# Performance work log

Measured on AMD Instinct MI355X. Metric: run time of the kernel, lower is better.

Reference implementation:

```python
import jax, jax.numpy as jnp
import numpy as np

N_NODES = 50000
N_EDGES = 320000
B = 4096          # subgraph batch: users/items/subg nodes
IN_N = 64         # in_nfeats
IN_E = 16         # in_efeats
OUT_E = 2 * IN_E  # out_edge_feats = in_efeats*2
H = 4             # num_heads
D = 64            # latent dim per layer (latent_dim=[64,64])
L = 2             # num EGAT layers


def setup_inputs() -> dict:
    key = jax.random.key(0)
    ks = iter(jax.random.split(key, 48))
    def nrm(shape, s=0.05):
        return jax.random.normal(next(ks), shape, dtype=jnp.float32) * s
    inp = {}
    inp['x'] = jax.random.normal(next(ks), (N_NODES, IN_N), dtype=jnp.float32)
    inp['efeat'] = jax.random.normal(next(ks), (N_EDGES, IN_E), dtype=jnp.float32)
    inp['efeat2'] = jax.random.normal(next(ks), (N_EDGES, IN_N), dtype=jnp.float32)
    inp['edge_mask'] = (jax.random.uniform(next(ks), (N_EDGES,)) > 0.1).astype(jnp.float32)
    inp['edge_mask2'] = (jax.random.uniform(next(ks), (N_EDGES,)) > 0.1).astype(jnp.float32)
    inp['src'] = jax.random.randint(next(ks), (N_EDGES,), 0, N_NODES, dtype=jnp.int32)
    inp['dst'] = jax.random.randint(next(ks), (N_EDGES,), 0, N_NODES, dtype=jnp.int32)
    inp['user_idx'] = jnp.arange(0, B, dtype=jnp.int32)          # ntype==0
    inp['item_idx'] = jnp.arange(B, 2 * B, dtype=jnp.int32)      # ntype==1
    inp['subg_idx'] = jnp.arange(2 * B, 3 * B, dtype=jnp.int32)  # ntype==-1
    # stacked per-layer EGAT params (layer dims identical since IN_N == D)
    inp['loc_wni'] = nrm((L, D, H * OUT_E))
    inp['loc_wnj'] = nrm((L, D, H * OUT_E))
    inp['loc_we'] = nrm((L, IN_E, H * OUT_E))
    inp['loc_attn'] = nrm((L, H, OUT_E))
    inp['loc_wnode'] = nrm((L, D, H * D))
    inp['agg1_w'] = nrm((L, H * D, D))
    inp['agg1_b'] = jnp.zeros((L, D), jnp.float32)
    inp['glob_wni'] = nrm((L, D, H * OUT_E))
    inp['glob_wnj'] = nrm((L, D, H * OUT_E))
    inp['glob_we'] = nrm((L, IN_N, H * OUT_E))
    inp['glob_attn'] = nrm((L, H, OUT_E))
    inp['glob_wnode'] = nrm((L, D, H * D))
    inp['agg2_w'] = nrm((L, H * D, D))
    inp['agg2_b'] = jnp.zeros((L, D), jnp.float32)
    inp['w1_ui'] = nrm((2 * L * D, 128))
    inp['b1_ui'] = jnp.zeros((128,), jnp.float32)
    inp['w1_sg'] = nrm((L * D, 128))
    inp['b1_sg'] = jnp.zeros((128,), jnp.float32)
    inp['w2_ui'] = nrm((128, 1))
    inp['b2_ui'] = jnp.zeros((1,), jnp.float32)
    inp['w2_sg'] = nrm((128, 1))
    inp['b2_sg'] = jnp.zeros((1,), jnp.float32)
    return inp


def _egat(x, e, norm, src, dst, wni, wnj, we, attn, wnode):
    # edge feature: f_ij = LeakyReLU(W_ni x_i + W_nj x_j + W_e e_ij), slope 0.2 (DGL EGATConv)
    f = (x @ wni)[src] + (x @ wnj)[dst] + e @ we            # (E, H*OUT_E)
    f = jax.nn.leaky_relu(f.reshape(-1, H, OUT_E), 0.2)
    scores = jnp.einsum('ehd,hd->eh', f, attn)              # (E, H)
    # edge softmax over incoming edges of each dst node
    m = jax.ops.segment_max(scores, dst, num_segments=N_NODES)
    m = jnp.where(jnp.isfinite(m), m, 0.0)
    ex = jnp.exp(scores - m[dst])
    denom = jax.ops.segment_sum(ex, dst, num_segments=N_NODES)
    a = ex / (denom[dst] + 1e-9)
    a = a * norm[:, None]                                    # per-edge norm (edge mask) weighting
    fn = (x @ wnode).reshape(-1, H, D)                       # (N, H, D)
    msg = fn[src] * a[:, :, None]                            # (E, H, D)
    out = jax.ops.segment_sum(msg, dst, num_segments=N_NODES)
    return out, a


def reference(x, efeat, efeat2, edge_mask, edge_mask2, src, dst, user_idx, item_idx, subg_idx,
              loc_wni, loc_wnj, loc_we, loc_attn, loc_wnode, agg1_w, agg1_b,
              glob_wni, glob_wnj, glob_we, glob_attn, glob_wnode, agg2_w, agg2_b,
              w1_ui, b1_ui, w1_sg, b1_sg, w2_ui, b2_ui, w2_sg, b2_sg):
    h = x
    ui_states, sg_states = [], []
    for l in range(L):
        out, _ = _egat(h, efeat, edge_mask, src, dst,
                       loc_wni[l], loc_wnj[l], loc_we[l], loc_attn[l], loc_wnode[l])
        h = jax.nn.elu(out.reshape(N_NODES, H * D) @ agg1_w[l] + agg1_b[l])
        ui_states.append(h)
        out, _ = _egat(h, efeat2, edge_mask2, src, dst,
                       glob_wni[l], glob_wnj[l], glob_we[l], glob_attn[l], glob_wnode[l])
        h = jax.nn.leaky_relu(out.reshape(N_NODES, H * D) @ agg2_w[l] + agg2_b[l], 0.01)
        sg_states.append(h)
    ui = jnp.concatenate(ui_states, axis=1)   # (N, L*D)
    sg = jnp.concatenate(sg_states, axis=1)   # (N, L*D)
    ui_x = jnp.concatenate([ui[user_idx], ui[item_idx]], axis=1)  # (B, 2*L*D)
    sg_x = sg[subg_idx]                                           # (B, L*D)
    ui_h = jax.nn.relu(ui_x @ w1_ui + b1_ui)  # dropout is identity in eval
    sg_h = jax.nn.relu(sg_x @ w1_sg + b1_sg)
    ui_out = jax.nn.sigmoid(ui_h @ w2_ui + b2_ui)[:, 0]
    sg_out = jax.nn.sigmoid(sg_h @ w2_sg + b2_sg)[:, 0]
    return (sg_out, ui_out)
```

## Files before the change

### kernel.cpp

```cpp
#include <hip/hip_runtime.h>
#include <math.h>

#define NN 50000
#define NE 320000
#define BATCH 4096

typedef __bf16 bf16x8 __attribute__((ext_vector_type(8)));
typedef float floatx4 __attribute__((ext_vector_type(4)));
typedef unsigned short ushort;
typedef unsigned int uint;

__device__ __forceinline__ float lrelu02(float x) { return x > 0.f ? x : 0.2f * x; }
__device__ __forceinline__ float b2f(ushort h) { return __uint_as_float(((uint)h) << 16); }
__device__ __forceinline__ float b2f_lo(uint u) { return __uint_as_float(u << 16); }
__device__ __forceinline__ float b2f_hi(uint u) { return __uint_as_float(u & 0xffff0000u); }
__device__ __forceinline__ ushort f2b(float x) {
    uint u = __float_as_uint(x);
    return (ushort)((u + 0x7fffu + ((u >> 16) & 1u)) >> 16);
}
__device__ __forceinline__ uint pk2(float a, float b) {
    return (uint)f2b(a) | ((uint)f2b(b) << 16);
}

template <int GLOB>
__global__ __launch_bounds__(512, 6) void score_frag(
    const float* __restrict__ ef,
    const ushort* __restrict__ Bfrag,
    const ushort* __restrict__ hb,
    const int* __restrict__ srcv, const int* __restrict__ dstv,
    const int* __restrict__ pos,
    const float* __restrict__ attn, float* __restrict__ scv)
{
    constexpr int KTOT = GLOB ? 192 : 160;
    constexpr int NR = KTOT / 32;
    constexpr int EFR = GLOB ? 2 : 1;
    constexpr int LDA = GLOB ? 64 : 16;
    __shared__ __align__(16) ushort As[128 * KTOT];
    const int tid = threadIdx.x;
    const int w = tid >> 6, lane = tid & 63;
    const int quad = lane >> 4, l16 = lane & 15;
    const int row = (blockIdx.x << 7) + 16 * w + l16;

    const int s_n = srcv[row];
    const int d_n = dstv[row];
    const int prow = pos[row];

    bf16x8 bfr[NR];
#pragma unroll
    for (int rnd = 0; rnd < EFR; rnd++) {
        uint4 av = make_uint4(0u, 0u, 0u, 0u);
        int k0 = rnd * 32 + quad * 8;
        if (GLOB || quad < 2) {
            const float* ap = ef + (size_t)row * LDA + k0;
            float4 f0 = *(const float4*)ap;
            float4 f1 = *(const float4*)(ap + 4);
            av.x = pk2(f0.x, f0.y);
            av.y = pk2(f0.z, f0.w);
            av.z = pk2(f1.x, f1.y);
            av.w = pk2(f1.z, f1.w);
        }
        *(uint4*)&bfr[rnd] = av;
    }
#pragma unroll
    for (int rr = 0; rr < 2; rr++)
        bfr[EFR + rr] = *(const bf16x8*)(hb + (size_t)s_n * 64 + rr * 32 + quad * 8);
#pragma unroll
    for (int rr = 0; rr < 2; rr++)
        bfr[EFR + 2 + rr] = *(const bf16x8*)(hb + (size_t)d_n * 64 + rr * 32 + quad * 8);

    for (int i = tid; i < 128 * KTOT / 8; i += 512)
        *(uint4*)(As + (size_t)i * 8) = *(const uint4*)(Bfrag + (size_t)i * 8);
    __syncthreads();

    floatx4 acc[8];
#pragma unroll
    for (int c = 0; c < 8; c++)
#pragma unroll
        for (int r = 0; r < 4; r++) acc[c][r] = 0.f;

#pragma unroll
    for (int rnd = 0; rnd < NR; rnd++) {
#pragma unroll
        for (int c = 0; c < 8; c++) {
            bf16x8 afr = *(const bf16x8*)(As + ((size_t)(c * NR + rnd) * 64 + lane) * 8);
            acc[c] = __builtin_amdgcn_mfma_f32_16x16x32_bf16(afr, bfr[rnd], acc[c], 0, 0, 0);
        }
    }

    float ph[4] = {0.f, 0.f, 0.f, 0.f};
#pragma unroll
    for (int c = 0; c < 8; c++) {
        int fbase = 16 * c + quad * 4;
        float4 at4 = *(const float4*)(attn + fbase);
        float v = lrelu02(acc[c][0]) * at4.x;
        v = fmaf(lrelu02(acc[c][1]), at4.y, v);
        v = fmaf(lrelu02(acc[c][2]), at4.z, v);
        v = fmaf(lrelu02(acc[c][3]), at4.w, v);
        ph[fbase >> 5] += v;
    }
#pragma unroll
    for (int h = 0; h < 4; h++) {
        ph[h] += __shfl_xor(ph[h], 16);
        ph[h] += __shfl_xor(ph[h], 32);
    }
    if (quad == 0)
        *(float4*)(scv + (size_t)prow * 4) = make_float4(ph[0], ph[1], ph[2], ph[3]);
}

__global__ __launch_bounds__(256) void gemm_agg(
    const ushort* __restrict__ A, int M,
    const ushort* __restrict__ Bt,
    const float* __restrict__ bias, int act,
    ushort* __restrict__ outb)
{
    __shared__ __align__(16) ushort As[64 * 32];
    __shared__ __align__(16) ushort Bs[64 * 32];
    const int tid = threadIdx.x;
    const int row0 = blockIdx.x << 6;
    const int w = tid >> 6, lane = tid & 63;
    const int quad = lane >> 4, l16 = lane & 15;
    const int arow = tid >> 2, c0 = (tid & 3) << 3;
    const int agrow = row0 + arow;

    floatx4 acc[4];
#pragma unroll
    for (int c = 0; c < 4; c++)
#pragma unroll
        for (int r = 0; r < 4; r++) acc[c][r] = 0.f;

    for (int kt = 0; kt < 256; kt += 32) {
        uint4 av = make_uint4(0u, 0u, 0u, 0u);
        if (agrow < M)
            av = *(const uint4*)(A + (size_t)agrow * 256 + kt + c0);
        *(uint4*)(As + arow * 32 + c0) = av;
        {
            int bn = tid >> 2, bk = (tid & 3) << 3;
            *(uint4*)(Bs + bn * 32 + bk) = *(const uint4*)(Bt + (size_t)bn * 256 + kt + bk);
        }
        __syncthreads();
        bf16x8 af = *(const bf16x8*)(As + (16 * w + l16) * 32 + quad * 8);
#pragma unroll
        for (int c = 0; c < 4; c++) {
            bf16x8 bfv = *(const bf16x8*)(Bs + (16 * c + l16) * 32 + quad * 8);
            acc[c] = __builtin_amdgcn_mfma_f32_16x16x32_bf16(af, bfv, acc[c], 0, 0, 0);
        }
        if (kt + 32 < 256) __syncthreads();
    }
#pragma unroll
    for (int r = 0; r < 4; r++) {
        int gr = row0 + 16 * w + quad * 4 + r;
        if (gr < M) {
#pragma unroll
            for (int c = 0; c < 4; c++) {
                int col = 16 * c + l16;
                float v = acc[c][r] + bias[col];
                if (act == 0) v = v > 0.f ? v : (__expf(v) - 1.f);
                else          v = v > 0.f ? v : 0.01f * v;
                outb[(size_t)gr * 64 + col] = f2b(v);
            }
        }
    }
}

__global__ void k_count(const int* __restrict__ dst, int* __restrict__ deg, int E)
{
    for (int i = blockIdx.x * blockDim.x + threadIdx.x; i < E; i += gridDim.x * blockDim.x)
        atomicAdd(&deg[dst[i]], 1);
}

__global__ __launch_bounds__(256) void scan_local(
    const int* __restrict__ deg, int* __restrict__ rowptr, int* __restrict__ partials, int N)
{
    __shared__ int sd[256];
    int tid = threadIdx.x;
    int i = blockIdx.x * 256 + tid;
    int v = (i < N) ? deg[i] : 0;
    sd[tid] = v; __syncthreads();
#pragma unroll
    for (int off = 1; off < 256; off <<= 1) {
        int t = (tid >= off) ? sd[tid - off] : 0;
        __syncthreads();
        sd[tid] += t;
        __syncthreads();
    }
    if (i < N) rowptr[i] = sd[tid] - v;
    if (tid == 255) partials[blockIdx.x] = sd[255];
}

__global__ __launch_bounds__(256) void scan_partials(int* __restrict__ partials, int nb)
{
    __shared__ int sd[256];
    int tid = threadIdx.x;
    int v = (tid < nb) ? partials[tid] : 0;
    sd[tid] = v; __syncthreads();
#pragma unroll
    for (int off = 1; off < 256; off <<= 1) {
        int t = (tid >= off) ? sd[tid - off] : 0;
        __syncthreads();
        sd[tid] += t;
        __syncthreads();
    }
    if (tid < nb) partials[tid] = sd[tid] - v;
}

__global__ void scan_add(int* __restrict__ rowptr, const int* __restrict__ partials, int N, int E)
{
    int i = blockIdx.x * 256 + threadIdx.x;
    if (i < N) rowptr[i] += partials[i >> 8];
    if (i == 0) rowptr[N] = E;
}

__global__ void k_scatter(const int* __restrict__ dst, const int* __restrict__ rowptr,
                          int* __restrict__ cnt, int* __restrict__ eidx, int E)
{
    for (int i = blockIdx.x * blockDim.x + threadIdx.x; i < E; i += gridDim.x * blockDim.x) {
        int d = dst[i];
        int p = rowptr[d] + atomicAdd(&cnt[d], 1);
        eidx[p] = i;
    }
}

__global__ void k_sort_buckets(const int* __restrict__ rowptr, int* __restrict__ eidx, int N)
{
    int n = blockIdx.x * blockDim.x + threadIdx.x;
    if (n >= N) return;
    int beg = rowptr[n], end = rowptr[n + 1];
    for (int i = beg + 1; i < end; i++) {
        int v = eidx[i];
        int j = i - 1;
        while (j >= beg && eidx[j] > v) { eidx[j + 1] = eidx[j]; j--; }
        eidx[j + 1] = v;
    }
}

__global__ void k_perm_small(const int* __restrict__ eidx, const int* __restrict__ src,
                             const float* __restrict__ m1, const float* __restrict__ m2,
                             int* __restrict__ srcp, float* __restrict__ m1p,
                             float* __restrict__ m2p, int* __restrict__ pos, int E)
{
    int p = blockIdx.x * blockDim.x + threadIdx.x;
    if (p < E) {
        int e = eidx[p];
        srcp[p] = src[e];
        m1p[p] = m1[e];
        m2p[p] = m2[e];
        pos[e] = p;
    }
}

__global__ void k_cvt(const float* __restrict__ in, ushort* __restrict__ out, int n)
{
    for (int i = blockIdx.x * blockDim.x + threadIdx.x; i < n; i += gridDim.x * blockDim.x)
        out[i] = f2b(in[i]);
}

__global__ void k_prep_score_all(const float* __restrict__ loc_we, const float* __restrict__ glob_we,
                                 const float* __restrict__ loc_wni, const float* __restrict__ glob_wni,
                                 const float* __restrict__ loc_wnj, const float* __restrict__ glob_wnj,
                                 ushort* __restrict__ B)
{
    int idx = blockIdx.x * 256 + threadIdx.x;
    if (idx >= 4 * 24576) return;
    int e = idx / 24576, rem = idx % 24576;
    int layer = e >> 1, gl = e & 1;
    int KTOT = gl ? 192 : 160;
    int NR = KTOT / 32;
    int ef_end = gl ? 64 : 32;
    int ef_real = gl ? 64 : 16;
    if (rem >= 128 * KTOT) return;
    int j = rem & 7, lane = (rem >> 3) & 63, t = rem >> 9;
    int c = t / NR, rnd = t % NR;
    int m = 16 * c + (lane & 15);
    int k = 32 * rnd + (lane >> 4) * 8 + j;
    const float* we  = (gl ? glob_we  + layer * 64 * 128 : loc_we  + layer * 16 * 128);
    const float* wni = (gl ? glob_wni : loc_wni) + layer * 64 * 128;
    const float* wnj = (gl ? glob_wnj : loc_wnj) + layer * 64 * 128;
    float v;
    if (k < ef_end)            v = (k < ef_real) ? we[k * 128 + m] : 0.f;
    else if (k < ef_end + 64)  v = wni[(k - ef_end) * 128 + m];
    else                       v = wnj[(k - ef_end - 64) * 128 + m];
    B[e * 24576 + rem] = f2b(v);
}

__global__ void k_fold_all(const float* __restrict__ loc_wnode, const float* __restrict__ agg1_w,
                           const float* __restrict__ glob_wnode, const float* __restrict__ agg2_w,
                           ushort* __restrict__ B)
{
    int e = blockIdx.x >> 6;
    int idx = (blockIdx.x & 63) * 256 + threadIdx.x;
    int layer = e >> 1, gl = e & 1;
    const float* wnode = (gl ? glob_wnode : loc_wnode) + layer * 64 * 256;
    const float* aggw  = (gl ? agg2_w : agg1_w) + layer * 256 * 64;
    int j = idx >> 8, col = idx & 255;
    int h = col >> 6, ii = col & 63;
    float s = 0.f;
#pragma unroll 8
    for (int k = 0; k < 64; k++)
        s = fmaf(wnode[ii * 256 + h * 64 + k], aggw[(h * 64 + k) * 64 + j], s);
    B[e * 16384 + j * 256 + col] = f2b(s);
}

__global__ __launch_bounds__(256) void node_fused(
    const float* __restrict__ scv,
    const int* __restrict__ rowptr, const int* __restrict__ srcp,
    const float* __restrict__ maskp,
    const ushort* __restrict__ hsrc,
    ushort* __restrict__ zb)
{
    int tid = threadIdx.x;
    int n = (blockIdx.x << 4) | (tid >> 4);
    int sl = tid & 15;
    int beg = rowptr[n], end = rowptr[n + 1];
    float l0 = 0.f, l1 = 0.f, l2 = 0.f, l3 = 0.f;
    float acc[4][4] = {};
#pragma unroll 2
    for (int i = beg; i < end; i++) {
        float4 s4 = *(const float4*)(scv + (size_t)i * 4);
        float mk = maskp[i];
        int s = srcp[i];
        uint2 hvv = *(const uint2*)(hsrc + (size_t)s * 64 + sl * 4);
        float t0 = __expf(s4.x), t1 = __expf(s4.y), t2 = __expf(s4.z), t3 = __expf(s4.w);
        l0 += t0; l1 += t1; l2 += t2; l3 += t3;
        float a0 = t0 * mk, a1 = t1 * mk, a2 = t2 * mk, a3 = t3 * mk;
        float hv[4] = { b2f_lo(hvv.x), b2f_hi(hvv.x), b2f_lo(hvv.y), b2f_hi(hvv.y) };
#pragma unroll
        for (int c = 0; c < 4; c++) {
            acc[0][c] = fmaf(a0, hv[c], acc[0][c]);
            acc[1][c] = fmaf(a1, hv[c], acc[1][c]);
            acc[2][c] = fmaf(a2, hv[c], acc[2][c]);
            acc[3][c] = fmaf(a3, hv[c], acc[3][c]);
        }
    }
    float inv[4] = { 1.f / (l0 + 1e-9f), 1.f / (l1 + 1e-9f),
                     1.f / (l2 + 1e-9f), 1.f / (l3 + 1e-9f) };
#pragma unroll
    for (int h = 0; h < 4; h++) {
        uint2 o;
        o.x = (uint)f2b(acc[h][0] * inv[h]) | ((uint)f2b(acc[h][1] * inv[h]) << 16);
        o.y = (uint)f2b(acc[h][2] * inv[h]) | ((uint)f2b(acc[h][3] * inv[h]) << 16);
        *(uint2*)(zb + (size_t)n * 256 + h * 64 + sl * 4) = o;
    }
}

__global__ __launch_bounds__(256) void final_ui(
    const ushort* __restrict__ s0, const ushort* __restrict__ s1,
    const int* __restrict__ uidx, const int* __restrict__ iidx,
    const float* __restrict__ w1, const float* __restrict__ b1,
    const float* __restrict__ w2, const float* __restrict__ b2, float* __restrict__ out)
{
    __shared__ float xs[4][256];
    int tid = threadIdx.x, wid = tid >> 6, lane = tid & 63;
    int r = (blockIdx.x << 2) + wid;
    int u = uidx[r], it = iidx[r];
    xs[wid][lane]       = b2f(s0[(size_t)u * 64 + lane]);
    xs[wid][64 + lane]  = b2f(s1[(size_t)u * 64 + lane]);
    xs[wid][128 + lane] = b2f(s0[(size_t)it * 64 + lane]);
    xs[wid][192 + lane] = b2f(s1[(size_t)it * 64 + lane]);
    __syncthreads();
    int c = lane << 1;
    float a0 = b1[c], a1 = b1[c + 1];
    for (int k = 0; k < 256; k++) {
        float xv = xs[wid][k];
        float2 wv = *(const float2*)(w1 + (size_t)k * 128 + c);
        a0 = fmaf(xv, wv.x, a0);
        a1 = fmaf(xv, wv.y, a1);
    }
    a0 = fmaxf(a0, 0.f);
    a1 = fmaxf(a1, 0.f);
    float2 w2v = *(const float2*)(w2 + c);
    float p = a0 * w2v.x + a1 * w2v.y;
#pragma unroll
    for (int mm = 1; mm < 64; mm <<= 1) p += __shfl_xor(p, mm);
    if (lane == 0) out[r] = 1.f / (1.f + __expf(-(p + b2[0])));
}

__global__ __launch_bounds__(256) void final_sg(
    const ushort* __restrict__ s0, const ushort* __restrict__ s1,
    const int* __restrict__ gidx,
    const float* __restrict__ w1, const float* __restrict__ b1,
    const float* __restrict__ w2, const float* __restrict__ b2, float* __restrict__ out)
{
    __shared__ float xs[4][128];
    int tid = threadIdx.x, wid = tid >> 6, lane = tid & 63;
    int r = (blockIdx.x << 2) + wid;
    int n = gidx[r];
    xs[wid][lane]      = b2f(s0[(size_t)n * 64 + lane]);
    xs[wid][64 + lane] = b2f(s1[(size_t)n * 64 + lane]);
    __syncthreads();
    int c = lane << 1;
    float a0 = b1[c], a1 = b1[c + 1];
    for (int k = 0; k < 128; k++) {
        float xv = xs[wid][k];
        float2 wv = *(const float2*)(w1 + (size_t)k * 128 + c);
        a0 = fmaf(xv, wv.x, a0);
        a1 = fmaf(xv, wv.y, a1);
    }
    a0 = fmaxf(a0, 0.f);
    a1 = fmaxf(a1, 0.f);
    float2 w2v = *(const float2*)(w2 + c);
    float p = a0 * w2v.x + a1 * w2v.y;
#pragma unroll
    for (int mm = 1; mm < 64; mm <<= 1) p += __shfl_xor(p, mm);
    if (lane == 0) out[r] = 1.f / (1.f + __expf(-(p + b2[0])));
}

extern "C" void kernel_launch(void* const* d_in, const int* in_sizes, int n_in,
                              void* d_out, int out_size, void* d_ws, size_t ws_size,
                              hipStream_t stream)
{
    const float* x       = (const float*)d_in[0];
    const float* efeat   = (const float*)d_in[1];
    const float* efeat2  = (const float*)d_in[2];
    const float* mask1   = (const float*)d_in[3];
    const float* mask2   = (const float*)d_in[4];
    const int*   src     = (const int*)d_in[5];
    const int*   dst     = (const int*)d_in[6];
    const int*   uidx    = (const int*)d_in[7];
    const int*   iidx    = (const int*)d_in[8];
    const int*   gidx    = (const int*)d_in[9];
    const float* loc_wni = (const float*)d_in[10];
    const float* loc_wnj = (const float*)d_in[11];
    const float* loc_we  = (const float*)d_in[12];
    const float* loc_attn= (const float*)d_in[13];
    const float* loc_wnode=(const float*)d_in[14];
    const float* agg1_w  = (const float*)d_in[15];
    const float* agg1_b  = (const float*)d_in[16];
    const float* glob_wni= (const float*)d_in[17];
    const float* glob_wnj= (const float*)d_in[18];
    const float* glob_we = (const float*)d_in[19];
    const float* glob_attn=(const float*)d_in[20];
    const float* glob_wnode=(const float*)d_in[21];
    const float* agg2_w  = (const float*)d_in[22];
    const float* agg2_b  = (const float*)d_in[23];
    const float* w1_ui   = (const float*)d_in[24];
    const float* b1_ui   = (const float*)d_in[25];
    const float* w1_sg   = (const float*)d_in[26];
    const float* b1_sg   = (const float*)d_in[27];
    const float* w2_ui   = (const float*)d_in[28];
    const float* b2_ui   = (const float*)d_in[29];
    const float* w2_sg   = (const float*)d_in[30];
    const float* b2_sg   = (const float*)d_in[31];

    char* wsp = (char*)d_ws;
    auto carve = [&](size_t bytes) { char* p = wsp; wsp += (bytes + 255) & ~(size_t)255; return p; };
    ushort* zb    = (ushort*)carve((size_t)NN * 256 * 2);
    ushort* hb[5];
    for (int i = 0; i < 5; i++) hb[i] = (ushort*)carve((size_t)NN * 64 * 2);
    float*  scv   = (float*)carve((size_t)NE * 16);
    float*  m1p   = (float*)carve((size_t)NE * 4);
    float*  m2p   = (float*)carve((size_t)NE * 4);
    int*    srcp  = (int*)carve((size_t)NE * 4);
    int*    pos   = (int*)carve((size_t)NE * 4);
    int*    eidx  = (int*)carve((size_t)NE * 4);
    ushort* Bsc   = (ushort*)carve(4 * 24576 * 2);
    ushort* Bfold = (ushort*)carve(4 * 16384 * 2);
    int* deg      = (int*)carve(NN * 4);
    int* rowptr   = (int*)carve((NN + 4) * 4);
    int* partials = (int*)carve(256 * 4);

    k_prep_score_all<<<384, 256, 0, stream>>>(loc_we, glob_we, loc_wni, glob_wni,
                                              loc_wnj, glob_wnj, Bsc);
    k_fold_all<<<256, 256, 0, stream>>>(loc_wnode, agg1_w, glob_wnode, agg2_w, Bfold);
    hipMemsetAsync(deg, 0, NN * sizeof(int), stream);
    k_count<<<1280, 256, 0, stream>>>(dst, deg, NE);
    scan_local<<<196, 256, 0, stream>>>(deg, rowptr, partials, NN);
    scan_partials<<<1, 256, 0, stream>>>(partials, 196);
    scan_add<<<196, 256, 0, stream>>>(rowptr, partials, NN, NE);
    hipMemsetAsync(deg, 0, NN * sizeof(int), stream);
    k_scatter<<<1280, 256, 0, stream>>>(dst, rowptr, deg, eidx, NE);
    k_sort_buckets<<<196, 256, 0, stream>>>(rowptr, eidx, NN);
    k_perm_small<<<1250, 256, 0, stream>>>(eidx, src, mask1, mask2,
                                           srcp, m1p, m2p, pos, NE);
    k_cvt<<<3200, 256, 0, stream>>>(x, hb[0], NN * 64);

    auto egat = [&](const ushort* hin, int e, const float* maskp, const float* attn,
                    const float* aggb, int act, ushort* hout) {
        int is_glob = e & 1;
        if (is_glob)
            score_frag<1><<<2500, 512, 0, stream>>>(efeat2, Bsc + e * 24576, hin,
                                                    src, dst, pos, attn, scv);
        else
            score_frag<0><<<2500, 512, 0, stream>>>(efeat, Bsc + e * 24576, hin,
                                                    src, dst, pos, attn, scv);
        node_fused<<<NN / 16, 256, 0, stream>>>(scv, rowptr, srcp, maskp, hin, zb);
        gemm_agg<<<782, 256, 0, stream>>>(zb, NN, Bfold + e * 16384, aggb, act, hout);
    };

    egat(hb[0], 0, m1p, loc_attn,        agg1_b,      0, hb[1]);
    egat(hb[1], 1, m2p, glob_attn,       agg2_b,      1, hb[2]);
    egat(hb[2], 2, m1p, loc_attn + 128,  agg1_b + 64, 0, hb[3]);
    egat(hb[3], 3, m2p, glob_attn + 128, agg2_b + 64, 1, hb[4]);

    float* out = (float*)d_out;
    final_sg<<<BATCH / 4, 256, 0, stream>>>(hb[2], hb[4], gidx, w1_sg, b1_sg, w2_sg, b2_sg, out);
    final_ui<<<BATCH / 4, 256, 0, stream>>>(hb[1], hb[3], uidx, iidx, w1_ui, b1_ui, w2_ui, b2_ui, out + BATCH);
}
```

Baseline: 588.6 us.

## Switch edge scoring to 32x32x16 MFMA and read scores via eidx indirection

The edge score kernel now uses 32x32x16 bf16 MFMA tiles with 256 edges per block instead of 16x16x32 tiles with 128. This removes the zero-padded K for the local edge features (K 144 instead of 160). Scores are written in original edge order, so the pos array and its scattered writes go away. The node aggregation kernel now gathers scores through eidx, which turns the earlier scattered writes into scattered reads. Occupancy drops to 4 waves per SIMD because the larger accumulators need more registers.

After: 560.8 us. 4.7% less time.

```diff
diff --git a/kernel.cpp b/kernel.cpp
--- a/kernel.cpp
+++ b/kernel.cpp
@@ -7,6 +7,7 @@
 
 typedef __bf16 bf16x8 __attribute__((ext_vector_type(8)));
 typedef float floatx4 __attribute__((ext_vector_type(4)));
+typedef float floatx16 __attribute__((ext_vector_type(16)));
 typedef unsigned short ushort;
 typedef unsigned int uint;
 
@@ -23,88 +24,74 @@
 }
 
 template <int GLOB>
-__global__ __launch_bounds__(512, 6) void score_frag(
+__global__ __launch_bounds__(512, 4) void score32(
     const float* __restrict__ ef,
     const ushort* __restrict__ Bfrag,
     const ushort* __restrict__ hb,
     const int* __restrict__ srcv, const int* __restrict__ dstv,
-    const int* __restrict__ pos,
     const float* __restrict__ attn, float* __restrict__ scv)
 {
-    constexpr int KTOT = GLOB ? 192 : 160;
-    constexpr int NR = KTOT / 32;
-    constexpr int EFR = GLOB ? 2 : 1;
+    constexpr int NK = GLOB ? 12 : 9;
+    constexpr int KTOT = NK * 16;
+    constexpr int EFR = GLOB ? 4 : 1;
     constexpr int LDA = GLOB ? 64 : 16;
     __shared__ __align__(16) ushort As[128 * KTOT];
     const int tid = threadIdx.x;
-    const int w = tid >> 6, lane = tid & 63;
-    const int quad = lane >> 4, l16 = lane & 15;
-    const int row = (blockIdx.x << 7) + 16 * w + l16;
+    const int wid = tid >> 6, lane = tid & 63;
+    const int hi = lane >> 5;
+    const int row = (blockIdx.x << 8) + (wid << 5) + (lane & 31);
 
     const int s_n = srcv[row];
     const int d_n = dstv[row];
-    const int prow = pos[row];
-
-    bf16x8 bfr[NR];
-#pragma unroll
-    for (int rnd = 0; rnd < EFR; rnd++) {
-        uint4 av = make_uint4(0u, 0u, 0u, 0u);
-        int k0 = rnd * 32 + quad * 8;
-        if (GLOB || quad < 2) {
-            const float* ap = ef + (size_t)row * LDA + k0;
-            float4 f0 = *(const float4*)ap;
-            float4 f1 = *(const float4*)(ap + 4);
-            av.x = pk2(f0.x, f0.y);
-            av.y = pk2(f0.z, f0.w);
-            av.z = pk2(f1.x, f1.y);
-            av.w = pk2(f1.z, f1.w);
-        }
-        *(uint4*)&bfr[rnd] = av;
-    }
-#pragma unroll
-    for (int rr = 0; rr < 2; rr++)
-        bfr[EFR + rr] = *(const bf16x8*)(hb + (size_t)s_n * 64 + rr * 32 + quad * 8);
-#pragma unroll
-    for (int rr = 0; rr < 2; rr++)
-        bfr[EFR + 2 + rr] = *(const bf16x8*)(hb + (size_t)d_n * 64 + rr * 32 + quad * 8);
+
+    bf16x8 bfr[NK];
+#pragma unroll
+    for (int t = 0; t < EFR; t++) {
+        const float* ap = ef + (size_t)row * LDA + t * 16 + hi * 8;
+        float4 f0 = *(const float4*)ap;
+        float4 f1 = *(const float4*)(ap + 4);
+        uint4 av;
+        av.x = pk2(f0.x, f0.y); av.y = pk2(f0.z, f0.w);
+        av.z = pk2(f1.x, f1.y); av.w = pk2(f1.z, f1.w);
+        *(uint4*)&bfr[t] = av;
+    }
+#pragma unroll
+    for (int t = 0; t < 4; t++)
+        bfr[EFR + t] = *(const bf16x8*)(hb + (size_t)s_n * 64 + t * 16 + hi * 8);
+#pragma unroll
+    for (int t = 0; t < 4; t++)
+        bfr[EFR + 4 + t] = *(const bf16x8*)(hb + (size_t)d_n * 64 + t * 16 + hi * 8);
 
     for (int i = tid; i < 128 * KTOT / 8; i += 512)
         *(uint4*)(As + (size_t)i * 8) = *(const uint4*)(Bfrag + (size_t)i * 8);
     __syncthreads();
 
-    floatx4 acc[8];
-#pragma unroll
-    for (int c = 0; c < 8; c++)
-#pragma unroll
-        for (int r = 0; r < 4; r++) acc[c][r] = 0.f;
-
-#pragma unroll
-    for (int rnd = 0; rnd < NR; rnd++) {
-#pragma unroll
-        for (int c = 0; c < 8; c++) {
-            bf16x8 afr = *(const bf16x8*)(As + ((size_t)(c * NR + rnd) * 64 + lane) * 8);
-            acc[c] = __builtin_amdgcn_mfma_f32_16x16x32_bf16(afr, bfr[rnd], acc[c], 0, 0, 0);
-        }
-    }
-
-    float ph[4] = {0.f, 0.f, 0.f, 0.f};
-#pragma unroll
-    for (int c = 0; c < 8; c++) {
-        int fbase = 16 * c + quad * 4;
-        float4 at4 = *(const float4*)(attn + fbase);
-        float v = lrelu02(acc[c][0]) * at4.x;
-        v = fmaf(lrelu02(acc[c][1]), at4.y, v);
-        v = fmaf(lrelu02(acc[c][2]), at4.z, v);
-        v = fmaf(lrelu02(acc[c][3]), at4.w, v);
-        ph[fbase >> 5] += v;
-    }
-#pragma unroll
-    for (int h = 0; h < 4; h++) {
-        ph[h] += __shfl_xor(ph[h], 16);
-        ph[h] += __shfl_xor(ph[h], 32);
-    }
-    if (quad == 0)
-        *(float4*)(scv + (size_t)prow * 4) = make_float4(ph[0], ph[1], ph[2], ph[3]);
+    float ph[4];
+#pragma unroll
+    for (int c = 0; c < 4; c++) {
+        floatx16 acc;
+#pragma unroll
+        for (int r = 0; r < 16; r++) acc[r] = 0.f;
+#pragma unroll
+        for (int t = 0; t < NK; t++) {
+            bf16x8 afr = *(const bf16x8*)(As + ((size_t)(c * NK + t) * 64 + lane) * 8);
+            acc = __builtin_amdgcn_mfma_f32_32x32x16_bf16(afr, bfr[t], acc, 0, 0, 0);
+        }
+        float v = 0.f;
+#pragma unroll
+        for (int q = 0; q < 4; q++) {
+            float4 at4 = *(const float4*)(attn + c * 32 + hi * 4 + q * 8);
+            v = fmaf(lrelu02(acc[q * 4 + 0]), at4.x, v);
+            v = fmaf(lrelu02(acc[q * 4 + 1]), at4.y, v);
+            v = fmaf(lrelu02(acc[q * 4 + 2]), at4.z, v);
+            v = fmaf(lrelu02(acc[q * 4 + 3]), at4.w, v);
+        }
+        ph[c] = v;
+    }
+#pragma unroll
+    for (int h = 0; h < 4; h++) ph[h] += __shfl_xor(ph[h], 32);
+    if (hi == 0)
+        *(float4*)(scv + (size_t)row * 4) = make_float4(ph[0], ph[1], ph[2], ph[3]);
 }
 
 __global__ __launch_bounds__(256) void gemm_agg(
@@ -236,7 +223,7 @@
 __global__ void k_perm_small(const int* __restrict__ eidx, const int* __restrict__ src,
                              const float* __restrict__ m1, const float* __restrict__ m2,
                              int* __restrict__ srcp, float* __restrict__ m1p,
-                             float* __restrict__ m2p, int* __restrict__ pos, int E)
+                             float* __restrict__ m2p, int E)
 {
     int p = blockIdx.x * blockDim.x + threadIdx.x;
     if (p < E) {
@@ -244,7 +231,6 @@
         srcp[p] = src[e];
         m1p[p] = m1[e];
         m2p[p] = m2[e];
-        pos[e] = p;
     }
 }
 
@@ -263,20 +249,19 @@
     if (idx >= 4 * 24576) return;
     int e = idx / 24576, rem = idx % 24576;
     int layer = e >> 1, gl = e & 1;
-    int KTOT = gl ? 192 : 160;
-    int NR = KTOT / 32;
-    int ef_end = gl ? 64 : 32;
-    int ef_real = gl ? 64 : 16;
+    int NK = gl ? 12 : 9;
+    int KTOT = NK * 16;
+    int ef_end = gl ? 64 : 16;
     if (rem >= 128 * KTOT) return;
-    int j = rem & 7, lane = (rem >> 3) & 63, t = rem >> 9;
-    int c = t / NR, rnd = t % NR;
-    int m = 16 * c + (lane & 15);
-    int k = 32 * rnd + (lane >> 4) * 8 + j;
+    int j = rem & 7, lane = (rem >> 3) & 63, tf = rem >> 9;
+    int c = tf / NK, t = tf % NK;
+    int m = 32 * c + (lane & 31);
+    int k = 16 * t + 8 * (lane >> 5) + j;
     const float* we  = (gl ? glob_we  + layer * 64 * 128 : loc_we  + layer * 16 * 128);
     const float* wni = (gl ? glob_wni : loc_wni) + layer * 64 * 128;
     const float* wnj = (gl ? glob_wnj : loc_wnj) + layer * 64 * 128;
     float v;
-    if (k < ef_end)            v = (k < ef_real) ? we[k * 128 + m] : 0.f;
+    if (k < ef_end)            v = we[k * 128 + m];
     else if (k < ef_end + 64)  v = wni[(k - ef_end) * 128 + m];
     else                       v = wnj[(k - ef_end - 64) * 128 + m];
     B[e * 24576 + rem] = f2b(v);
@@ -302,6 +287,7 @@
 
 __global__ __launch_bounds__(256) void node_fused(
     const float* __restrict__ scv,
+    const int* __restrict__ eidx,
     const int* __restrict__ rowptr, const int* __restrict__ srcp,
     const float* __restrict__ maskp,
     const ushort* __restrict__ hsrc,
@@ -315,7 +301,8 @@
     float acc[4][4] = {};
 #pragma unroll 2
     for (int i = beg; i < end; i++) {
-        float4 s4 = *(const float4*)(scv + (size_t)i * 4);
+        int ep = eidx[i];
+        float4 s4 = *(const float4*)(scv + (size_t)ep * 4);
         float mk = maskp[i];
         int s = srcp[i];
         uint2 hvv = *(const uint2*)(hsrc + (size_t)s * 64 + sl * 4);
@@ -450,7 +437,6 @@
     float*  m1p   = (float*)carve((size_t)NE * 4);
     float*  m2p   = (float*)carve((size_t)NE * 4);
     int*    srcp  = (int*)carve((size_t)NE * 4);
-    int*    pos   = (int*)carve((size_t)NE * 4);
     int*    eidx  = (int*)carve((size_t)NE * 4);
     ushort* Bsc   = (ushort*)carve(4 * 24576 * 2);
     ushort* Bfold = (ushort*)carve(4 * 16384 * 2);
@@ -470,19 +456,19 @@
     k_scatter<<<1280, 256, 0, stream>>>(dst, rowptr, deg, eidx, NE);
     k_sort_buckets<<<196, 256, 0, stream>>>(rowptr, eidx, NN);
     k_perm_small<<<1250, 256, 0, stream>>>(eidx, src, mask1, mask2,
-                                           srcp, m1p, m2p, pos, NE);
+                                           srcp, m1p, m2p, NE);
     k_cvt<<<3200, 256, 0, stream>>>(x, hb[0], NN * 64);
 
     auto egat = [&](const ushort* hin, int e, const float* maskp, const float* attn,
                     const float* aggb, int act, ushort* hout) {
         int is_glob = e & 1;
         if (is_glob)
-            score_frag<1><<<2500, 512, 0, stream>>>(efeat2, Bsc + e * 24576, hin,
-                                                    src, dst, pos, attn, scv);
+            score32<1><<<1250, 512, 0, stream>>>(efeat2, Bsc + e * 24576, hin,
+                                                 src, dst, attn, scv);
         else
-            score_frag<0><<<2500, 512, 0, stream>>>(efeat, Bsc + e * 24576, hin,
-                                                    src, dst, pos, attn, scv);
-        node_fused<<<NN / 16, 256, 0, stream>>>(scv, rowptr, srcp, maskp, hin, zb);
+            score32<0><<<1250, 512, 0, stream>>>(efeat, Bsc + e * 24576, hin,
+                                                 src, dst, attn, scv);
+        node_fused<<<NN / 16, 256, 0, stream>>>(scv, eidx, rowptr, srcp, maskp, hin, zb);
         gemm_agg<<<782, 256, 0, stream>>>(zb, NN, Bfold + e * 16384, aggb, act, hout);
     };
 
```
